# Kernel optimization log

Measured on AMD Instinct MI355X. Metric: run time of the kernel, lower is better.

Reference implementation:

```python
import jax, jax.numpy as jnp
import numpy as np

D_MODEL = 1024
N_HEAD = 16
D_HEAD = D_MODEL // N_HEAD
B, S = 4, 2048


def setup_inputs() -> dict:
    key = jax.random.key(0)
    ks = jax.random.split(key, 10)
    def xavier(k, shape):
        fan_in, fan_out = shape[1], shape[0]
        limit = np.sqrt(6.0 / (fan_in + fan_out))
        return jax.random.uniform(k, shape, jnp.float32, -limit, limit)
    x = jax.random.normal(ks[0], (B, S, D_MODEL), jnp.float32)
    mask = jnp.tril(jnp.ones((S, S), jnp.int32))[None, None]  # causal [1,1,S,S]
    return {
        "x": x,
        "Wq": xavier(ks[1], (D_MODEL, D_MODEL)), "bq": jnp.zeros((D_MODEL,), jnp.float32),
        "Wk": xavier(ks[2], (D_MODEL, D_MODEL)), "bk": jnp.zeros((D_MODEL,), jnp.float32),
        "Wv": xavier(ks[3], (D_MODEL, D_MODEL)), "bv": jnp.zeros((D_MODEL,), jnp.float32),
        "Wo": xavier(ks[4], (D_MODEL, D_MODEL)), "bo": jnp.zeros((D_MODEL,), jnp.float32),
        "mask": mask,
    }


def reference(x, Wq, bq, Wk, bk, Wv, bv, Wo, bo, mask):
    b, s, d = x.shape
    # Linear layers use y = x @ W.T + b (torch convention)
    def proj(W, bias):
        y = jnp.einsum('bsd,ed->bse', x, W) + bias
        return y.reshape(b, s, N_HEAD, D_HEAD).transpose(0, 2, 1, 3)  # [B,H,S,Dh]
    q = proj(Wq, bq)
    k = proj(Wk, bk)
    v = proj(Wv, bv)
    scores = jnp.einsum('bhqd,bhkd->bhqk', q, k) / jnp.sqrt(jnp.float32(D_HEAD))
    scores = jnp.where(mask == 0, jnp.float32(-1e9), scores)
    attn = jax.nn.softmax(scores, axis=-1)  # dropout is identity at eval
    context = jnp.einsum('bhqk,bhkd->bhqd', attn, v)
    context = context.transpose(0, 2, 1, 3).reshape(b, s, d)
    return jnp.einsum('bsd,ed->bse', context, Wo) + bo
```

## Files before the change

### kernel.cpp

```cpp
#include <hip/hip_runtime.h>
#include <stdint.h>

#define D_MODEL 1024
#define NHEAD   16
#define DHEAD   64
#define BATCH   4
#define SEQ     2048
#define MTOT    (BATCH*SEQ)

typedef __attribute__((ext_vector_type(4))) float f32x4;
typedef __attribute__((ext_vector_type(8))) short bf16x8;

typedef __attribute__((address_space(3))) uint32_t lds_u32;
typedef const __attribute__((address_space(1))) uint32_t glb_u32;

__device__ static inline void gload_lds16(const void* g, void* l) {
    __builtin_amdgcn_global_load_lds((glb_u32*)g, (lds_u32*)l, 16, 0, 0);
}

__device__ static inline ushort f2bf(float f) {
    uint32_t u = __builtin_bit_cast(uint32_t, f);
    u += 0x7fffu + ((u >> 16) & 1u);
    return (ushort)(u >> 16);
}

__device__ static inline float exp2_fast(float x) {
    float r; asm("v_exp_f32 %0, %1" : "=v"(r) : "v"(x)); return r;
}
__device__ static inline uint32_t cvt_pk_bf16(float a, float b) {
    uint32_t r;
    asm("v_cvt_pk_bf16_f32 %0, %1, %2" : "=v"(r) : "v"(a), "v"(b));
    return r;
}

__global__ __launch_bounds__(256) void convert_kernel(
    const float4* __restrict__ x,
    const float4* __restrict__ wq, const float4* __restrict__ wk,
    const float4* __restrict__ wv, const float4* __restrict__ wo,
    ushort4* __restrict__ xb, ushort4* __restrict__ wb)
{
    const int NX4 = (MTOT * D_MODEL) / 4;
    const int NW4 = (D_MODEL * D_MODEL) / 4;
    const int TOT = NX4 + 4 * NW4;
    for (int i = blockIdx.x * blockDim.x + threadIdx.x; i < TOT;
         i += gridDim.x * blockDim.x) {
        float4 v; ushort4* dst;
        if (i < NX4) { v = x[i]; dst = &xb[i]; }
        else {
            int j = i - NX4;
            int w = j >> 18;
            int r = j & (NW4 - 1);
            const float4* s = (w == 0) ? wq : (w == 1) ? wk : (w == 2) ? wv : wo;
            v = s[r]; dst = &wb[(size_t)w * NW4 + r];
        }
        ushort4 o;
        o.x = f2bf(v.x); o.y = f2bf(v.y); o.z = f2bf(v.z); o.w = f2bf(v.w);
        *dst = o;
    }
}

template<int LAYOUT>
__global__ __launch_bounds__(256) void gemm_bt(
    const ushort* __restrict__ A,
    const ushort* __restrict__ W,
    const float*  __restrict__ bias,
    void* __restrict__ out, float scale)
{
    __shared__ __align__(16) ushort As[128 * 32];
    __shared__ __align__(16) ushort Bs[128 * 32];

    const int tid = threadIdx.x;
    const int w  = tid >> 6, l = tid & 63, lo = l & 15, hi = l >> 4;
    const int wr = w >> 1, wc = w & 1;

    const int id = blockIdx.y * 8 + blockIdx.x;
    const int mb = ((id & 7) << 3) | ((id >> 3) & 7);
    const int nb = id >> 6;
    const int m0 = mb * 128, n0 = nb * 128;

    f32x4 acc[4][4] = {};

    const int srow = l >> 2;
    const int sk   = (l & 3) * 8;

    for (int kt = 0; kt < 32; ++kt) {
        const int k0 = kt * 32;
        __syncthreads();
#pragma unroll
        for (int c = 0; c < 2; ++c) {
            const int row = c * 64 + w * 16 + srow;
            gload_lds16(&A[(size_t)(m0 + row) * 1024 + k0 + sk],
                        &As[(c * 64 + w * 16) * 32]);
            gload_lds16(&W[(size_t)(n0 + row) * 1024 + k0 + sk],
                        &Bs[(c * 64 + w * 16) * 32]);
        }
        __syncthreads();

        bf16x8 af[4], bfr[4];
#pragma unroll
        for (int mi = 0; mi < 4; ++mi)
            af[mi] = *(const bf16x8*)&As[(wr * 64 + mi * 16 + lo) * 32 + hi * 8];
#pragma unroll
        for (int ni = 0; ni < 4; ++ni)
            bfr[ni] = *(const bf16x8*)&Bs[(wc * 64 + ni * 16 + lo) * 32 + hi * 8];
#pragma unroll
        for (int mi = 0; mi < 4; ++mi)
#pragma unroll
            for (int ni = 0; ni < 4; ++ni)
                acc[mi][ni] = __builtin_amdgcn_mfma_f32_16x16x32_bf16(
                    af[mi], bfr[ni], acc[mi][ni], 0, 0, 0);
    }

#pragma unroll
    for (int mi = 0; mi < 4; ++mi) {
#pragma unroll
        for (int ni = 0; ni < 4; ++ni) {
            const int gj = n0 + wc * 64 + ni * 16 + lo;
            const float bj = bias[gj];
            if (LAYOUT == 0) {
#pragma unroll
                for (int r = 0; r < 4; ++r) {
                    const int gi = m0 + wr * 64 + mi * 16 + hi * 4 + r;
                    const int b = gi >> 11, s = gi & (SEQ - 1);
                    const int h = gj >> 6, dh = gj & 63;
                    ((ushort*)out)[(((size_t)(b * NHEAD + h)) * SEQ + s) * DHEAD + dh] =
                        f2bf((acc[mi][ni][r] + bj) * scale);
                }
            } else if (LAYOUT == 1) {
                const int gi0 = m0 + wr * 64 + mi * 16 + hi * 4;
                const int b = gi0 >> 11, s = gi0 & (SEQ - 1);
                const int h = gj >> 6, dh = gj & 63;
                ushort4 o4;
                o4.x = f2bf((acc[mi][ni][0] + bj) * scale);
                o4.y = f2bf((acc[mi][ni][1] + bj) * scale);
                o4.z = f2bf((acc[mi][ni][2] + bj) * scale);
                o4.w = f2bf((acc[mi][ni][3] + bj) * scale);
                *(ushort4*)&((ushort*)out)[(((size_t)(b * NHEAD + h)) * DHEAD + dh) * SEQ + s] = o4;
            } else {
#pragma unroll
                for (int r = 0; r < 4; ++r) {
                    const int gi = m0 + wr * 64 + mi * 16 + hi * 4 + r;
                    ((float*)out)[(size_t)gi * D_MODEL + gj] = (acc[mi][ni][r] + bj) * scale;
                }
            }
        }
    }
}

__global__ __launch_bounds__(256) void attn_kernel(
    const ushort* __restrict__ Q, const ushort* __restrict__ K,
    const ushort* __restrict__ Vt, ushort* __restrict__ ctx)
{
    __shared__ __align__(16) ushort Ks[64 * 64];
    __shared__ __align__(16) ushort Vs[64 * 64];
    __shared__ __align__(16) ushort Pq[4 * 32 * 64];

    const int tid = threadIdx.x;
    const int w = tid >> 6, l = tid & 63, lo = l & 15, hi = l >> 4;
    const int sw = lo & 7;

    const int fid = blockIdx.x;
    const int xcd = fid & 7;
    const int u = fid >> 3;
    const int g = xcd * 8 + (u & 7);
    const int b = g >> 4, h = g & 15;
    const int j = u >> 3;
    const size_t base = (size_t)(b * NHEAD + h) * SEQ * DHEAD;

    const int krow = tid >> 3;
    const int kcol = (tid & 7) * 8;
    char* PqW = (char*)&Pq[w * 2048];

    for (int pass = 0; pass < 2; ++pass) {
        const int qt = pass ? (15 - j) : j;
        const int q0 = qt << 7;
        const int qw0 = q0 + w * 32;

        bf16x8 qf[2][2];
#pragma unroll
        for (int mi = 0; mi < 2; ++mi)
#pragma unroll
            for (int ks = 0; ks < 2; ++ks)
                qf[mi][ks] = *(const bf16x8*)&Q[base +
                    (size_t)(qw0 + mi * 16 + lo) * DHEAD + ks * 32 + hi * 8];

        f32x4 o[2][4] = {};
        float mrow[2] = {-1e30f, -1e30f}, lrow[2] = {0.f, 0.f};

        const int ntiles = (q0 + 128) >> 6;
        bf16x8 kreg[2], vreg[2];
#pragma unroll
        for (int c = 0; c < 2; ++c) {
            kreg[c] = *(const bf16x8*)&K[base + (size_t)(c * 32 + krow) * DHEAD + kcol];
            vreg[c] = *(const bf16x8*)&Vt[base + (size_t)(c * 32 + krow) * SEQ + kcol];
        }

        for (int t = 0; t < ntiles; ++t) {
            const int kv0 = t << 6;
            __syncthreads();
#pragma unroll
            for (int c = 0; c < 2; ++c) {
                const int row = c * 32 + krow;
                const int g16 = (tid & 7) ^ (row & 7);
                *(bf16x8*)((char*)Ks + row * 128 + (g16 << 4)) = kreg[c];
                *(bf16x8*)((char*)Vs + row * 128 + (g16 << 4)) = vreg[c];
            }
            __syncthreads();
            if (t + 1 < ntiles) {
                const int nv0 = kv0 + 64;
#pragma unroll
                for (int c = 0; c < 2; ++c) {
                    kreg[c] = *(const bf16x8*)&K[base + (size_t)(nv0 + c * 32 + krow) * DHEAD + kcol];
                    vreg[c] = *(const bf16x8*)&Vt[base + (size_t)(c * 32 + krow) * SEQ + nv0 + kcol];
                }
            }
            if (kv0 > qw0 + 31) continue;

            f32x4 s[2][4] = {};
#pragma unroll
            for (int ks = 0; ks < 2; ++ks) {
                bf16x8 kf[4];
#pragma unroll
                for (int nj = 0; nj < 4; ++nj)
                    kf[nj] = *(const bf16x8*)((char*)Ks + (nj * 16 + lo) * 128 +
                                              ((((ks << 2) + hi) ^ sw) << 4));
#pragma unroll
                for (int mi = 0; mi < 2; ++mi)
#pragma unroll
                    for (int nj = 0; nj < 4; ++nj)
                        s[mi][nj] = __builtin_amdgcn_mfma_f32_16x16x32_bf16(
                            kf[nj], qf[mi][ks], s[mi][nj], 0, 0, 0);
            }

            if (kv0 + 63 > qw0) {
#pragma unroll
                for (int mi = 0; mi < 2; ++mi) {
                    const int gq = qw0 + mi * 16 + lo;
#pragma unroll
                    for (int nj = 0; nj < 4; ++nj)
#pragma unroll
                        for (int r = 0; r < 4; ++r) {
                            const int gk = kv0 + nj * 16 + hi * 4 + r;
                            if (gk > gq) s[mi][nj][r] = -1e30f;
                        }
                }
            }

            float tl[2], corr[2];
#pragma unroll
            for (int mi = 0; mi < 2; ++mi) {
                float m = s[mi][0][0];
#pragma unroll
                for (int nj = 0; nj < 4; ++nj)
#pragma unroll
                    for (int r = 0; r < 4; ++r) m = fmaxf(m, s[mi][nj][r]);
                tl[mi] = m;
            }
            const bool grow = (tl[0] > mrow[0] + 8.f) | (tl[1] > mrow[1] + 8.f);
            if (__any(grow)) {
#pragma unroll
                for (int mi = 0; mi < 2; ++mi) {
                    float m2 = fmaxf(tl[mi], __shfl_xor(tl[mi], 16));
                    m2 = fmaxf(m2, __shfl_xor(m2, 32));
                    const float mn = fmaxf(mrow[mi], m2);
                    corr[mi] = exp2_fast(mrow[mi] - mn);
                    mrow[mi] = mn;
                }
#pragma unroll
                for (int mi = 0; mi < 2; ++mi)
#pragma unroll
                    for (int r = 0; r < 4; ++r) {
                        const float cb = __shfl(corr[mi], hi * 4 + r);
#pragma unroll
                        for (int ni = 0; ni < 4; ++ni) o[mi][ni][r] *= cb;
                    }
            } else { corr[0] = 1.f; corr[1] = 1.f; }

#pragma unroll
            for (int mi = 0; mi < 2; ++mi) {
                float ls = 0.f;
#pragma unroll
                for (int nj = 0; nj < 4; ++nj) {
#pragma unroll
                    for (int r = 0; r < 4; ++r) {
                        const float p = exp2_fast(s[mi][nj][r] - mrow[mi]);
                        s[mi][nj][r] = p;
                        ls += p;
                    }
                    uint2 pp;
                    pp.x = cvt_pk_bf16(s[mi][nj][0], s[mi][nj][1]);
                    pp.y = cvt_pk_bf16(s[mi][nj][2], s[mi][nj][3]);
                    const int gP = ((nj << 1) + (hi >> 1)) ^ sw;
                    *(uint2*)(PqW + (mi * 16 + lo) * 128 + (gP << 4) + ((hi & 1) << 3)) = pp;
                }
                ls += __shfl_xor(ls, 16);
                ls += __shfl_xor(ls, 32);
                lrow[mi] = lrow[mi] * corr[mi] + ls;
            }

#pragma unroll
            for (int ks2 = 0; ks2 < 2; ++ks2) {
                bf16x8 pf[2], vf[4];
#pragma unroll
                for (int mi = 0; mi < 2; ++mi)
                    pf[mi] = *(const bf16x8*)(PqW + (mi * 16 + lo) * 128 +
                                              ((((ks2 << 2) + hi) ^ sw) << 4));
#pragma unroll
                for (int ni = 0; ni < 4; ++ni)
                    vf[ni] = *(const bf16x8*)((char*)Vs + (ni * 16 + lo) * 128 +
                                              ((((ks2 << 2) + hi) ^ sw) << 4));
#pragma unroll
                for (int mi = 0; mi < 2; ++mi)
#pragma unroll
                    for (int ni = 0; ni < 4; ++ni)
                        o[mi][ni] = __builtin_amdgcn_mfma_f32_16x16x32_bf16(
                            pf[mi], vf[ni], o[mi][ni], 0, 0, 0);
            }
        }

#pragma unroll
        for (int mi = 0; mi < 2; ++mi) {
            const float rv = 1.0f / lrow[mi];
#pragma unroll
            for (int r = 0; r < 4; ++r) {
                const float rb = __shfl(rv, hi * 4 + r);
                const int gq = qw0 + mi * 16 + hi * 4 + r;
#pragma unroll
                for (int ni = 0; ni < 4; ++ni)
                    ctx[((size_t)(b * SEQ + gq)) * D_MODEL + h * DHEAD + ni * 16 + lo] =
                        f2bf(o[mi][ni][r] * rb);
            }
        }
    }
}

extern "C" void kernel_launch(void* const* d_in, const int* in_sizes, int n_in,
                              void* d_out, int out_size, void* d_ws, size_t ws_size,
                              hipStream_t stream) {
    const float* x  = (const float*)d_in[0];
    const float* Wq = (const float*)d_in[1];
    const float* bq = (const float*)d_in[2];
    const float* Wk = (const float*)d_in[3];
    const float* bk = (const float*)d_in[4];
    const float* Wv = (const float*)d_in[5];
    const float* bv = (const float*)d_in[6];
    const float* Wo = (const float*)d_in[7];
    const float* bo = (const float*)d_in[8];

    char* ws = (char*)d_ws;
    ushort* xb  = (ushort*)(ws);
    ushort* wb  = (ushort*)(ws + (16u << 20));
    ushort* Qb  = (ushort*)(ws + (24u << 20));
    ushort* Kb  = (ushort*)(ws + (40u << 20));
    ushort* Vtb = (ushort*)(ws + (56u << 20));
    ushort* ctx = (ushort*)(ws + (72u << 20));

    convert_kernel<<<2048, 256, 0, stream>>>(
        (const float4*)x, (const float4*)Wq, (const float4*)Wk,
        (const float4*)Wv, (const float4*)Wo, (ushort4*)xb, (ushort4*)wb);

    const int NW = D_MODEL * D_MODEL;
    dim3 ggrid(D_MODEL / 128, MTOT / 128);
    const float qscale = 0.125f * 1.44269504f;
    gemm_bt<0><<<ggrid, 256, 0, stream>>>(xb, wb + 0 * NW, bq, Qb, qscale);
    gemm_bt<0><<<ggrid, 256, 0, stream>>>(xb, wb + 1 * NW, bk, Kb, 1.0f);
    gemm_bt<1><<<ggrid, 256, 0, stream>>>(xb, wb + 2 * NW, bv, Vtb, 1.0f);

    attn_kernel<<<512, 256, 0, stream>>>(Qb, Kb, Vtb, ctx);

    gemm_bt<2><<<ggrid, 256, 0, stream>>>(ctx, wb + 3 * NW, bo, (float*)d_out, 1.0f);
}
```

Baseline: 184.5 us.

## Fuse QKV projections into one GEMM launch, double-buffer KV prefetch, add MFMA priority

Merges the three Q/K/V projection GEMMs into a single 1536-block launch over the concatenated weight matrix, picking bias, scale and output layout per 1024-column region. The attention kernel now prefetches K/V tiles two steps ahead using two register buffers, and raises wave priority around the MFMA sections with s_setprio. The intent is to cut launch overhead, fill the GPU better in the projection step, and hide global-load latency in attention. The cost is more registers in attention, which could lower occupancy.

```diff
diff --git a/kernel.cpp b/kernel.cpp
--- a/kernel.cpp
+++ b/kernel.cpp
@@ -59,12 +59,98 @@
     }
 }
 
-template<int LAYOUT>
-__global__ __launch_bounds__(256) void gemm_bt(
+__global__ __launch_bounds__(256) void gemm_qkv(
+    const ushort* __restrict__ A,
+    const ushort* __restrict__ W3,
+    const float* __restrict__ bq, const float* __restrict__ bk,
+    const float* __restrict__ bv,
+    ushort* __restrict__ Qb, ushort* __restrict__ Kb, ushort* __restrict__ Vtb,
+    float qscale)
+{
+    __shared__ __align__(16) ushort As[128 * 32];
+    __shared__ __align__(16) ushort Bs[128 * 32];
+
+    const int tid = threadIdx.x;
+    const int w  = tid >> 6, l = tid & 63, lo = l & 15, hi = l >> 4;
+    const int wr = w >> 1, wc = w & 1;
+
+    const int id = blockIdx.x;
+    const int mb = ((id & 7) << 3) | ((id >> 3) & 7);
+    const int nb = id >> 6;
+    const int m0 = mb * 128, n0 = nb * 128;
+
+    f32x4 acc[4][4] = {};
+    const int srow = l >> 2;
+    const int sk   = (l & 3) * 8;
+
+    for (int kt = 0; kt < 32; ++kt) {
+        const int k0 = kt * 32;
+        __syncthreads();
+#pragma unroll
+        for (int c = 0; c < 2; ++c) {
+            const int row = c * 64 + w * 16 + srow;
+            gload_lds16(&A[(size_t)(m0 + row) * 1024 + k0 + sk],
+                        &As[(c * 64 + w * 16) * 32]);
+            gload_lds16(&W3[(size_t)(n0 + row) * 1024 + k0 + sk],
+                        &Bs[(c * 64 + w * 16) * 32]);
+        }
+        __syncthreads();
+
+        bf16x8 af[4], bfr[4];
+#pragma unroll
+        for (int mi = 0; mi < 4; ++mi)
+            af[mi] = *(const bf16x8*)&As[(wr * 64 + mi * 16 + lo) * 32 + hi * 8];
+#pragma unroll
+        for (int ni = 0; ni < 4; ++ni)
+            bfr[ni] = *(const bf16x8*)&Bs[(wc * 64 + ni * 16 + lo) * 32 + hi * 8];
+#pragma unroll
+        for (int mi = 0; mi < 4; ++mi)
+#pragma unroll
+            for (int ni = 0; ni < 4; ++ni)
+                acc[mi][ni] = __builtin_amdgcn_mfma_f32_16x16x32_bf16(
+                    af[mi], bfr[ni], acc[mi][ni], 0, 0, 0);
+    }
+
+    const int region = nb >> 3;
+    const float scale = (region == 0) ? qscale : 1.0f;
+    const float* bias = (region == 0) ? bq : (region == 1) ? bk : bv;
+    ushort* outQK = (region == 0) ? Qb : Kb;
+
+#pragma unroll
+    for (int mi = 0; mi < 4; ++mi) {
+#pragma unroll
+        for (int ni = 0; ni < 4; ++ni) {
+            const int gj  = n0 + wc * 64 + ni * 16 + lo;
+            const int lcl = gj & 1023;
+            const int h = lcl >> 6, dh = lcl & 63;
+            const float bj = bias[lcl];
+            if (region < 2) {
+#pragma unroll
+                for (int r = 0; r < 4; ++r) {
+                    const int gi = m0 + wr * 64 + mi * 16 + hi * 4 + r;
+                    const int b = gi >> 11, s = gi & (SEQ - 1);
+                    outQK[(((size_t)(b * NHEAD + h)) * SEQ + s) * DHEAD + dh] =
+                        f2bf((acc[mi][ni][r] + bj) * scale);
+                }
+            } else {
+                const int gi0 = m0 + wr * 64 + mi * 16 + hi * 4;
+                const int b = gi0 >> 11, s = gi0 & (SEQ - 1);
+                ushort4 o4;
+                o4.x = f2bf(acc[mi][ni][0] + bj);
+                o4.y = f2bf(acc[mi][ni][1] + bj);
+                o4.z = f2bf(acc[mi][ni][2] + bj);
+                o4.w = f2bf(acc[mi][ni][3] + bj);
+                *(ushort4*)&Vtb[(((size_t)(b * NHEAD + h)) * DHEAD + dh) * SEQ + s] = o4;
+            }
+        }
+    }
+}
+
+__global__ __launch_bounds__(256) void gemm_out(
     const ushort* __restrict__ A,
     const ushort* __restrict__ W,
     const float*  __restrict__ bias,
-    void* __restrict__ out, float scale)
+    float* __restrict__ out)
 {
     __shared__ __align__(16) ushort As[128 * 32];
     __shared__ __align__(16) ushort Bs[128 * 32];
@@ -79,7 +165,6 @@
     const int m0 = mb * 128, n0 = nb * 128;
 
     f32x4 acc[4][4] = {};
-
     const int srow = l >> 2;
     const int sk   = (l & 3) * 8;
 
@@ -112,39 +197,17 @@
     }
 
 #pragma unroll
-    for (int mi = 0; mi < 4; ++mi) {
+    for (int mi = 0; mi < 4; ++mi)
 #pragma unroll
         for (int ni = 0; ni < 4; ++ni) {
             const int gj = n0 + wc * 64 + ni * 16 + lo;
             const float bj = bias[gj];
-            if (LAYOUT == 0) {
-#pragma unroll
-                for (int r = 0; r < 4; ++r) {
-                    const int gi = m0 + wr * 64 + mi * 16 + hi * 4 + r;
-                    const int b = gi >> 11, s = gi & (SEQ - 1);
-                    const int h = gj >> 6, dh = gj & 63;
-                    ((ushort*)out)[(((size_t)(b * NHEAD + h)) * SEQ + s) * DHEAD + dh] =
-                        f2bf((acc[mi][ni][r] + bj) * scale);
-                }
-            } else if (LAYOUT == 1) {
-                const int gi0 = m0 + wr * 64 + mi * 16 + hi * 4;
-                const int b = gi0 >> 11, s = gi0 & (SEQ - 1);
-                const int h = gj >> 6, dh = gj & 63;
-                ushort4 o4;
-                o4.x = f2bf((acc[mi][ni][0] + bj) * scale);
-                o4.y = f2bf((acc[mi][ni][1] + bj) * scale);
-                o4.z = f2bf((acc[mi][ni][2] + bj) * scale);
-                o4.w = f2bf((acc[mi][ni][3] + bj) * scale);
-                *(ushort4*)&((ushort*)out)[(((size_t)(b * NHEAD + h)) * DHEAD + dh) * SEQ + s] = o4;
-            } else {
-#pragma unroll
-                for (int r = 0; r < 4; ++r) {
-                    const int gi = m0 + wr * 64 + mi * 16 + hi * 4 + r;
-                    ((float*)out)[(size_t)gi * D_MODEL + gj] = (acc[mi][ni][r] + bj) * scale;
-                }
-            }
-        }
-    }
+#pragma unroll
+            for (int r = 0; r < 4; ++r) {
+                const int gi = m0 + wr * 64 + mi * 16 + hi * 4 + r;
+                out[(size_t)gi * D_MODEL + gj] = acc[mi][ni][r] + bj;
+            }
+        }
 }
 
 __global__ __launch_bounds__(256) void attn_kernel(
@@ -188,35 +251,39 @@
         float mrow[2] = {-1e30f, -1e30f}, lrow[2] = {0.f, 0.f};
 
         const int ntiles = (q0 + 128) >> 6;
-        bf16x8 kreg[2], vreg[2];
+        bf16x8 kreg[2][2], vreg[2][2];
 #pragma unroll
         for (int c = 0; c < 2; ++c) {
-            kreg[c] = *(const bf16x8*)&K[base + (size_t)(c * 32 + krow) * DHEAD + kcol];
-            vreg[c] = *(const bf16x8*)&Vt[base + (size_t)(c * 32 + krow) * SEQ + kcol];
+            kreg[0][c] = *(const bf16x8*)&K[base + (size_t)(c * 32 + krow) * DHEAD + kcol];
+            vreg[0][c] = *(const bf16x8*)&Vt[base + (size_t)(c * 32 + krow) * SEQ + kcol];
+            kreg[1][c] = *(const bf16x8*)&K[base + (size_t)(64 + c * 32 + krow) * DHEAD + kcol];
+            vreg[1][c] = *(const bf16x8*)&Vt[base + (size_t)(c * 32 + krow) * SEQ + 64 + kcol];
         }
 
         for (int t = 0; t < ntiles; ++t) {
             const int kv0 = t << 6;
+            const int pb = t & 1;
             __syncthreads();
 #pragma unroll
             for (int c = 0; c < 2; ++c) {
                 const int row = c * 32 + krow;
                 const int g16 = (tid & 7) ^ (row & 7);
-                *(bf16x8*)((char*)Ks + row * 128 + (g16 << 4)) = kreg[c];
-                *(bf16x8*)((char*)Vs + row * 128 + (g16 << 4)) = vreg[c];
+                *(bf16x8*)((char*)Ks + row * 128 + (g16 << 4)) = kreg[pb][c];
+                *(bf16x8*)((char*)Vs + row * 128 + (g16 << 4)) = vreg[pb][c];
             }
             __syncthreads();
-            if (t + 1 < ntiles) {
-                const int nv0 = kv0 + 64;
+            if (t + 2 < ntiles) {
+                const int nv0 = kv0 + 128;
 #pragma unroll
                 for (int c = 0; c < 2; ++c) {
-                    kreg[c] = *(const bf16x8*)&K[base + (size_t)(nv0 + c * 32 + krow) * DHEAD + kcol];
-                    vreg[c] = *(const bf16x8*)&Vt[base + (size_t)(c * 32 + krow) * SEQ + nv0 + kcol];
+                    kreg[pb][c] = *(const bf16x8*)&K[base + (size_t)(nv0 + c * 32 + krow) * DHEAD + kcol];
+                    vreg[pb][c] = *(const bf16x8*)&Vt[base + (size_t)(c * 32 + krow) * SEQ + nv0 + kcol];
                 }
             }
             if (kv0 > qw0 + 31) continue;
 
             f32x4 s[2][4] = {};
+            __builtin_amdgcn_s_setprio(1);
 #pragma unroll
             for (int ks = 0; ks < 2; ++ks) {
                 bf16x8 kf[4];
@@ -231,6 +298,7 @@
                         s[mi][nj] = __builtin_amdgcn_mfma_f32_16x16x32_bf16(
                             kf[nj], qf[mi][ks], s[mi][nj], 0, 0, 0);
             }
+            __builtin_amdgcn_s_setprio(0);
 
             if (kv0 + 63 > qw0) {
 #pragma unroll
@@ -298,6 +366,7 @@
                 lrow[mi] = lrow[mi] * corr[mi] + ls;
             }
 
+            __builtin_amdgcn_s_setprio(1);
 #pragma unroll
             for (int ks2 = 0; ks2 < 2; ++ks2) {
                 bf16x8 pf[2], vf[4];
@@ -316,6 +385,7 @@
                         o[mi][ni] = __builtin_amdgcn_mfma_f32_16x16x32_bf16(
                             pf[mi], vf[ni], o[mi][ni], 0, 0, 0);
             }
+            __builtin_amdgcn_s_setprio(0);
         }
 
 #pragma unroll
@@ -360,13 +430,11 @@
         (const float4*)Wv, (const float4*)Wo, (ushort4*)xb, (ushort4*)wb);
 
     const int NW = D_MODEL * D_MODEL;
-    dim3 ggrid(D_MODEL / 128, MTOT / 128);
     const float qscale = 0.125f * 1.44269504f;
-    gemm_bt<0><<<ggrid, 256, 0, stream>>>(xb, wb + 0 * NW, bq, Qb, qscale);
-    gemm_bt<0><<<ggrid, 256, 0, stream>>>(xb, wb + 1 * NW, bk, Kb, 1.0f);
-    gemm_bt<1><<<ggrid, 256, 0, stream>>>(xb, wb + 2 * NW, bv, Vtb, 1.0f);
+
+    gemm_qkv<<<1536, 256, 0, stream>>>(xb, wb, bq, bk, bv, Qb, Kb, Vtb, qscale);
 
     attn_kernel<<<512, 256, 0, stream>>>(Qb, Kb, Vtb, ctx);
 
-    gemm_bt<2><<<ggrid, 256, 0, stream>>>(ctx, wb + 3 * NW, bo, (float*)d_out, 1.0f);
-}
+    gemm_out<<<dim3(8, 64), 256, 0, stream>>>(ctx, wb + 3 * NW, bo, (float*)d_out);
+}
```

Result: slower. 699.1 us (+278.9%).
